# Kernel optimization log

Measured on AMD Instinct MI355X. Metric: run time of the kernel, lower is better.

The kernel has to match this reference:

```python
import jax, jax.numpy as jnp
import numpy as np

B_SZ, N_IN, N_CTX, UNITS, RANK = 4096, 4096, 512, 4096, 256


def setup_inputs() -> dict:
    key = jax.random.key(0)
    ks = jax.random.split(key, 8)
    inputs = jax.random.normal(ks[0], (B_SZ, N_IN), dtype=jnp.float32)
    context = jax.random.normal(ks[1], (B_SZ, N_CTX), dtype=jnp.float32)
    # Orthogonal-ish init approximated by scaled normals (math-equivalent shapes)
    U = jax.random.normal(ks[2], (N_IN, RANK), dtype=jnp.float32) / np.sqrt(N_IN)
    S = jax.random.uniform(ks[3], (RANK,), dtype=jnp.float32, minval=0.5, maxval=1.5)
    V = jax.random.normal(ks[4], (UNITS, RANK), dtype=jnp.float32) / np.sqrt(UNITS)
    W = jax.random.normal(ks[5], (N_CTX, RANK), dtype=jnp.float32) / np.sqrt(N_CTX)
    B = jnp.zeros((RANK,), dtype=jnp.float32)
    bias = jnp.zeros((UNITS,), dtype=jnp.float32)
    return {"inputs": inputs, "context": context, "U": U, "S": S, "V": V, "W": W, "B": B, "bias": bias}


def reference(inputs, context, U, S, V, W, B, bias):
    # chi[b,r] = sigmoid(context @ W + B)
    chi = jax.nn.sigmoid(context @ W + B)                  # [B, R]
    # Original: kernel[b,n,m] = sum_r U[n,r]*S[r]*chi[b,r]*V[m,r];
    # out[b,m] = sum_n x[b,n]*kernel[b,n,m]. Algebraically equal to:
    t = (inputs @ U) * (S * chi)                           # [B, R]
    out = t @ V.T + bias                                   # first '+ self.bias'
    out = out + bias                                       # 'outputs += self.bias' (use_bias=True)
    return jax.nn.relu(out)
```

## Files before the change

kernel.cpp:

```cpp
#include <hip/hip_runtime.h>

#define B_SZ 4096
#define N_IN 4096
#define N_CTX 512
#define UNITS 4096
#define RANK 256
#define ZSPLIT 16

typedef __attribute__((ext_vector_type(8))) __bf16 bf16x8;
typedef __attribute__((ext_vector_type(4))) float f32x4;
typedef __attribute__((ext_vector_type(8))) unsigned short ushort8;

__device__ __forceinline__ unsigned short f2bf(float f) {
    __bf16 h = (__bf16)f;
    return __builtin_bit_cast(unsigned short, h);
}
__device__ __forceinline__ float bf2f(unsigned short h) {
    return __uint_as_float(((unsigned int)h) << 16);
}
__device__ __forceinline__ void gload_lds16(const unsigned short* g, unsigned short* l) {
    __builtin_amdgcn_global_load_lds(
        (const __attribute__((address_space(1))) unsigned int*)g,
        (__attribute__((address_space(3))) unsigned int*)l, 16, 0, 0);
}
__device__ __forceinline__ bf16x8 ldfrag(const unsigned short* p) {
    ushort8 t = *(const ushort8*)p;
    return __builtin_bit_cast(bf16x8, t);
}

__global__ void prep(const float* __restrict__ U, const float* __restrict__ W,
                     const float* __restrict__ V,
                     unsigned short* __restrict__ UT, unsigned short* __restrict__ WT,
                     unsigned short* __restrict__ Vb) {
    __shared__ unsigned short t[64][66];
    int bid = blockIdx.x, tid = threadIdx.x;
    if (bid < 288) {
        const float* src; unsigned short* dst; int R, C, rb, cb;
        if (bid < 256) { src = U; dst = UT; R = N_IN; C = RANK; rb = (bid & 63) * 64; cb = (bid >> 6) * 64; }
        else { int b = bid - 256; src = W; dst = WT; R = N_CTX; C = RANK; rb = (b & 7) * 64; cb = (b >> 3) * 64; }
        int r = tid >> 4, c4 = (tid & 15) * 4;
        for (int i = 0; i < 4; i++) {
            float4 v = *(const float4*)(src + (size_t)(rb + r + i * 16) * C + cb + c4);
            t[r + i * 16][c4 + 0] = f2bf(v.x);
            t[r + i * 16][c4 + 1] = f2bf(v.y);
            t[r + i * 16][c4 + 2] = f2bf(v.z);
            t[r + i * 16][c4 + 3] = f2bf(v.w);
        }
        __syncthreads();
        int c = tid >> 3, r8 = (tid & 7) * 8;
        for (int j = 0; j < 2; j++) {
            int cc = c + j * 32;
            ushort8 o;
            for (int k = 0; k < 8; k++) o[k] = t[r8 + k][cc];
            *(ushort8*)(dst + (size_t)(cb + cc) * R + rb + r8) = o;
        }
    } else {
        size_t base = (size_t)(bid - 288) * 2048 + (size_t)tid * 8;
        float4 a = *(const float4*)(V + base);
        float4 b = *(const float4*)(V + base + 4);
        ushort8 o = { f2bf(a.x), f2bf(a.y), f2bf(a.z), f2bf(a.w),
                      f2bf(b.x), f2bf(b.y), f2bf(b.z), f2bf(b.w) };
        *(ushort8*)(Vb + base) = o;
    }
}


__launch_bounds__(512, 2)
__global__ void k21(const float* __restrict__ X, const unsigned short* __restrict__ UT,
                    unsigned short* __restrict__ T0p,
                    const float* __restrict__ ctx, const unsigned short* __restrict__ WT,
                    const float* __restrict__ S, const float* __restrict__ Bb,
                    unsigned short* __restrict__ Schi) {
    __shared__ char smem[49152];
    int tid = threadIdx.x, bfull = blockIdx.x;
    int w = tid >> 6, lane = tid & 63;
    int ln15 = lane & 15, quad = lane >> 4;
    if (bfull < 512) {
        int z = bfull >> 5, my = bfull & 31;
        unsigned short* As = (unsigned short*)smem;
        unsigned short* Bs = As + 128 * 64;
        int wr = w >> 2, wc = w & 3;
        int tm = my * 128;
        int kbase = z * (N_IN / ZSPLIT);
        f32x4 acc[4][4] = {};
        int arow = tid >> 2, acs0 = (tid & 3) * 2;
        const float* ag = X + (size_t)(tm + arow) * N_IN + kbase + acs0 * 8;
        unsigned short* al0 = As + arow * 64 + ((acs0 + 0) ^ (arow & 7)) * 8;
        unsigned short* al1 = As + arow * 64 + ((acs0 + 1) ^ (arow & 7)) * 8;
        int bl8 = lane >> 3, bcs = lane & 7;
        int bgc = (bcs ^ bl8) * 8;
        for (int kt = 0; kt < (N_IN / ZSPLIT) / 64; kt++) {
            int k0 = kt * 64;
            for (int c = 0; c < 4; c++) {
                int row = w * 32 + c * 8 + bl8;
                gload_lds16(UT + (size_t)row * N_IN + kbase + k0 + bgc, Bs + row * 64 + bcs * 8);
            }
            {
                float4 v0 = *(const float4*)(ag + k0);
                float4 v1 = *(const float4*)(ag + k0 + 4);
                float4 u0 = *(const float4*)(ag + k0 + 8);
                float4 u1 = *(const float4*)(ag + k0 + 12);
                ushort8 a8 = { f2bf(v0.x), f2bf(v0.y), f2bf(v0.z), f2bf(v0.w),
                               f2bf(v1.x), f2bf(v1.y), f2bf(v1.z), f2bf(v1.w) };
                ushort8 b8 = { f2bf(u0.x), f2bf(u0.y), f2bf(u0.z), f2bf(u0.w),
                               f2bf(u1.x), f2bf(u1.y), f2bf(u1.z), f2bf(u1.w) };
                *(ushort8*)al0 = a8;
                *(ushort8*)al1 = b8;
            }
            __syncthreads();
            for (int kh = 0; kh < 2; kh++) {
                int ch = kh * 4 + quad;
                int sw = (ch ^ (ln15 & 7)) * 8;
                bf16x8 af[4];
                for (int i = 0; i < 4; i++)
                    af[i] = ldfrag(As + (wr * 64 + i * 16 + ln15) * 64 + sw);
                for (int j = 0; j < 4; j++) {
                    bf16x8 b = ldfrag(Bs + (wc * 64 + j * 16 + ln15) * 64 + sw);
                    for (int i = 0; i < 4; i++)
                        acc[i][j] = __builtin_amdgcn_mfma_f32_16x16x32_bf16(af[i], b, acc[i][j], 0, 0, 0);
                }
            }
            __syncthreads();
        }
        unsigned short* P = T0p + (size_t)z * B_SZ * RANK;
        unsigned short* ep = (unsigned short*)smem;
        const int EPW = 280;
        int er = tid >> 3, ec0 = tid & 7;
        for (int h = 0; h < 2; h++) {
            if (wr == h) {
                for (int i = 0; i < 4; i++)
                    for (int j = 0; j < 4; j++)
                        for (int r = 0; r < 4; r++)
                            ep[(i * 16 + quad * 4 + r) * EPW + wc * 64 + j * 16 + ln15] = f2bf(acc[i][j][r]);
            }
            __syncthreads();
            for (int k = 0; k < 4; k++) {
                int chunk = ec0 + 8 * k;
                *(ushort8*)(P + (size_t)(tm + h * 64 + er) * RANK + chunk * 8) =
                    *(const ushort8*)(ep + er * EPW + chunk * 8);
            }
            __syncthreads();
        }
    } else {
        int hh = tid >> 8;
        int sb = (bfull - 512) * 2 + hh;
        int bx = sb & 3, by = sb >> 2;
        int t = tid & 255;
        int lw = t >> 6, llane = t & 63;
        int lln15 = llane & 15, lquad = llane >> 4;
        int wr = lw >> 1, wc = lw & 1;
        unsigned short* base = (unsigned short*)smem + hh * 6144;
        unsigned short* As = base;
        unsigned short* Bs = base + 32 * 64;
        int tm = by * 32, tn = bx * 64;
        f32x4 acc2[2] = {};
        int arow = t >> 3, acs = t & 7;
        const float* ag = ctx + (size_t)(tm + arow) * N_CTX + acs * 8;
        unsigned short* al = As + arow * 64 + (acs ^ (arow & 7)) * 8;
        int bl8 = llane >> 3, bcs = llane & 7;
        int bgc = (bcs ^ bl8) * 8;
        for (int kt = 0; kt < 8; kt++) {
            int k0 = kt * 64;
            for (int c = 0; c < 2; c++) {
                int row = lw * 16 + c * 8 + bl8;
                gload_lds16(WT + (size_t)(tn + row) * N_CTX + k0 + bgc, Bs + row * 64 + bcs * 8);
            }
            {
                float4 v0 = *(const float4*)(ag + k0);
                float4 v1 = *(const float4*)(ag + k0 + 4);
                ushort8 a8 = { f2bf(v0.x), f2bf(v0.y), f2bf(v0.z), f2bf(v0.w),
                               f2bf(v1.x), f2bf(v1.y), f2bf(v1.z), f2bf(v1.w) };
                *(ushort8*)al = a8;
            }
            __syncthreads();
            for (int kh = 0; kh < 2; kh++) {
                int ch = kh * 4 + lquad;
                bf16x8 af = ldfrag(As + (wr * 16 + lln15) * 64 + (ch ^ (lln15 & 7)) * 8);
                for (int j = 0; j < 2; j++) {
                    int row = wc * 32 + j * 16 + lln15;
                    bf16x8 bfr = ldfrag(Bs + row * 64 + (ch ^ (lln15 & 7)) * 8);
                    acc2[j] = __builtin_amdgcn_mfma_f32_16x16x32_bf16(af, bfr, acc2[j], 0, 0, 0);
                }
            }
            __syncthreads();
        }
        for (int j = 0; j < 2; j++) {
            int col = tn + wc * 32 + j * 16 + lln15;
            float sv = S[col], bv = Bb[col];
            for (int r = 0; r < 4; r++) {
                int row = tm + wr * 16 + lquad * 4 + r;
                float x = acc2[j][r] + bv;
                float chi = sv / (1.f + __expf(-x));
                Schi[(size_t)row * RANK + col] = f2bf(chi);
            }
        }
    }
}

__global__ void e_red(const unsigned short* __restrict__ T0p, const unsigned short* __restrict__ Schi,
                      unsigned short* __restrict__ T) {
    int i = blockIdx.x * 256 + threadIdx.x;
    const size_t stride = (size_t)B_SZ * RANK;
    float a[8] = {};
    for (int z = 0; z < ZSPLIT; z++) {
        ushort8 p = *(const ushort8*)(T0p + z * stride + (size_t)i * 8);
        for (int k = 0; k < 8; k++) a[k] += bf2f(p[k]);
    }
    ushort8 s = *(const ushort8*)(Schi + (size_t)i * 8);
    ushort8 o;
    for (int k = 0; k < 8; k++) o[k] = f2bf(a[k] * bf2f(s[k]));
    *(ushort8*)(T + (size_t)i * 8) = o;
}

__launch_bounds__(512, 1)
__global__ void k3_out(const unsigned short* __restrict__ T, const unsigned short* __restrict__ Vb,
                       const float* __restrict__ bias, float* __restrict__ out) {
    __shared__ char smem[163840];
    unsigned short* Bs = (unsigned short*)smem;
    unsigned short* A0 = (unsigned short*)(smem + 65536);
    unsigned short* A1 = A0 + 64 * 256;
    float* ep = (float*)(smem + 131072);
    int tid = threadIdx.x, w = tid >> 6, lane = tid & 63;
    int ln15 = lane & 15, quad = lane >> 4;
    int wr = w >> 2, wc = w & 3;
    int tn = blockIdx.x * 128;
    int tmg = blockIdx.y * 512;
    int lr2 = lane >> 5, lc16 = lane & 31;

    for (int i = 0; i < 8; i++) {
        int row = (w * 8 + i) * 2 + lr2;
        int g = (lc16 & 24) | ((lc16 & 7) ^ (row & 7));
        gload_lds16(Vb + (size_t)(tn + row) * RANK + g * 8, Bs + row * 256 + lc16 * 8);
    }
#define STAGE_A3(buf, step) do { \
    for (int i = 0; i < 4; i++) { \
        int row = (w * 4 + i) * 2 + lr2; \
        int g = (lc16 & 24) | ((lc16 & 7) ^ (row & 7)); \
        gload_lds16(T + (size_t)(tmg + (step) * 64 + row) * RANK + g * 8, \
                    (buf) + row * 256 + lc16 * 8); \
    } } while (0)
    STAGE_A3(A0, 0);
    float bv0 = 2.f * bias[tn + wc * 32 + ln15];
    float bv1 = 2.f * bias[tn + wc * 32 + 16 + ln15];
    unsigned short* cur = A0;
    unsigned short* nxt = A1;
    for (int t = 0; t < 8; t++) {
        STAGE_A3(nxt, (t + 1) & 7);
        asm volatile("s_waitcnt vmcnt(4)" ::: "memory");
        __builtin_amdgcn_s_barrier();
        __builtin_amdgcn_sched_barrier(0);
        f32x4 acc[2][2] = {};
        for (int kh = 0; kh < 8; kh++) {
            int c = kh * 4 + quad;
            bf16x8 af[2], bf[2];
            for (int i = 0; i < 2; i++) {
                int row = wr * 32 + i * 16 + ln15;
                int c16 = (c & 24) | ((c & 7) ^ (row & 7));
                af[i] = ldfrag(cur + row * 256 + c16 * 8);
            }
            for (int j = 0; j < 2; j++) {
                int row = wc * 32 + j * 16 + ln15;
                int c16 = (c & 24) | ((c & 7) ^ (row & 7));
                bf[j] = ldfrag(Bs + row * 256 + c16 * 8);
            }
            for (int i = 0; i < 2; i++)
                for (int j = 0; j < 2; j++)
                    acc[i][j] = __builtin_amdgcn_mfma_f32_16x16x32_bf16(af[i], bf[j], acc[i][j], 0, 0, 0);
        }
        for (int i = 0; i < 2; i++)
            for (int j = 0; j < 2; j++) {
                float bv = j ? bv1 : bv0;
                for (int r = 0; r < 4; r++)
                    ep[(wr * 32 + i * 16 + quad * 4 + r) * 128 + wc * 32 + j * 16 + ln15] =
                        fmaxf(acc[i][j][r] + bv, 0.f);
            }
        asm volatile("s_waitcnt lgkmcnt(0)" ::: "memory");
        __builtin_amdgcn_s_barrier();
        __builtin_amdgcn_sched_barrier(0);
        {
            int er = tid >> 3, ec = tid & 7;
            size_t orow = (size_t)(tmg + t * 64 + er) * UNITS + tn;
            for (int k = 0; k < 4; k++)
                *(float4*)(out + orow + (ec + k * 8) * 4) =
                    *(const float4*)(ep + er * 128 + (ec + k * 8) * 4);
        }
        __builtin_amdgcn_s_barrier();
        unsigned short* tmp = cur; cur = nxt; nxt = tmp;
    }
#undef STAGE_A3
}

extern "C" void kernel_launch(void* const* d_in, const int* in_sizes, int n_in,
                              void* d_out, int out_size, void* d_ws, size_t ws_size,
                              hipStream_t stream) {
    (void)in_sizes; (void)n_in; (void)out_size; (void)ws_size;
    const float* inputs  = (const float*)d_in[0];
    const float* context = (const float*)d_in[1];
    const float* U       = (const float*)d_in[2];
    const float* S       = (const float*)d_in[3];
    const float* V       = (const float*)d_in[4];
    const float* W       = (const float*)d_in[5];
    const float* Bb      = (const float*)d_in[6];
    const float* bias    = (const float*)d_in[7];
    float* out = (float*)d_out;

    char* ws = (char*)d_ws;
    size_t o = 0;
    unsigned short* UT   = (unsigned short*)(ws + o); o += (size_t)RANK * N_IN * 2;
    unsigned short* WT   = (unsigned short*)(ws + o); o += (size_t)RANK * N_CTX * 2;
    unsigned short* Vb   = (unsigned short*)(ws + o); o += (size_t)UNITS * RANK * 2;
    unsigned short* Schi = (unsigned short*)(ws + o); o += (size_t)B_SZ * RANK * 2;
    unsigned short* T    = (unsigned short*)(ws + o); o += (size_t)B_SZ * RANK * 2;
    unsigned short* T0p  = (unsigned short*)(ws + o); o += (size_t)ZSPLIT * B_SZ * RANK * 2;

    prep<<<800, 256, 0, stream>>>(U, W, V, UT, WT, Vb);
    k21<<<768, 512, 0, stream>>>(inputs, UT, T0p, context, WT, S, Bb, Schi);
    e_red<<<(B_SZ * RANK) / (256 * 8), 256, 0, stream>>>(T0p, Schi, T);
    k3_out<<<dim3(32, 8), 512, 0, stream>>>(T, Vb, bias, out);
}
```

Baseline: 176.5 us.

## Software-pipeline split-K GEMM with multi-buffered LDS and halve the K split

Rewrites the inputs@U split-K main loop as a software pipeline. B tiles are triple-buffered in LDS via direct global-to-LDS loads, and A tiles are double-buffered through registers with explicit vmcnt waits and raw barriers. MFMA priority is raised during compute. The K split drops from 16 to 8, so each block does twice the K work and the reduction has fewer partials to sum. The cost is 128KB of LDS per block at one block per CU, half as many GEMM blocks, and a fragile hand-written wait-count schedule.

```diff
diff --git a/kernel.cpp b/kernel.cpp
--- a/kernel.cpp
+++ b/kernel.cpp
@@ -5,7 +5,7 @@
 #define N_CTX 512
 #define UNITS 4096
 #define RANK 256
-#define ZSPLIT 16
+#define ZSPLIT 8
 
 typedef __attribute__((ext_vector_type(8))) __bf16 bf16x8;
 typedef __attribute__((ext_vector_type(4))) float f32x4;
@@ -26,6 +26,9 @@
 __device__ __forceinline__ bf16x8 ldfrag(const unsigned short* p) {
     ushort8 t = *(const ushort8*)p;
     return __builtin_bit_cast(bf16x8, t);
+}
+__device__ __forceinline__ void gld4(float4& d, const float* p) {
+    asm volatile("global_load_dwordx4 %0, %1, off" : "=v"(d) : "v"(p) : "memory");
 }
 
 __global__ void prep(const float* __restrict__ U, const float* __restrict__ W,
@@ -64,64 +67,111 @@
     }
 }
 
-
-__launch_bounds__(512, 2)
+__launch_bounds__(512, 1)
 __global__ void k21(const float* __restrict__ X, const unsigned short* __restrict__ UT,
                     unsigned short* __restrict__ T0p,
                     const float* __restrict__ ctx, const unsigned short* __restrict__ WT,
                     const float* __restrict__ S, const float* __restrict__ Bb,
                     unsigned short* __restrict__ Schi) {
-    __shared__ char smem[49152];
+    __shared__ char smem[131072];
     int tid = threadIdx.x, bfull = blockIdx.x;
     int w = tid >> 6, lane = tid & 63;
     int ln15 = lane & 15, quad = lane >> 4;
-    if (bfull < 512) {
-        int z = bfull >> 5, my = bfull & 31;
-        unsigned short* As = (unsigned short*)smem;
-        unsigned short* Bs = As + 128 * 64;
+    if (bfull < 256) {
+        int mblk = bfull & 31, z = bfull >> 5;
+        unsigned short* Bs = (unsigned short*)smem;
+        unsigned short* Al = Bs + 3 * 256 * 64;
         int wr = w >> 2, wc = w & 3;
-        int tm = my * 128;
+        int tm = mblk * 128;
         int kbase = z * (N_IN / ZSPLIT);
         f32x4 acc[4][4] = {};
+        int bl8 = lane >> 3, bcs = lane & 7;
+        int bgc = (bcs ^ bl8) * 8;
         int arow = tid >> 2, acs0 = (tid & 3) * 2;
         const float* ag = X + (size_t)(tm + arow) * N_IN + kbase + acs0 * 8;
-        unsigned short* al0 = As + arow * 64 + ((acs0 + 0) ^ (arow & 7)) * 8;
-        unsigned short* al1 = As + arow * 64 + ((acs0 + 1) ^ (arow & 7)) * 8;
-        int bl8 = lane >> 3, bcs = lane & 7;
-        int bgc = (bcs ^ bl8) * 8;
-        for (int kt = 0; kt < (N_IN / ZSPLIT) / 64; kt++) {
-            int k0 = kt * 64;
-            for (int c = 0; c < 4; c++) {
-                int row = w * 32 + c * 8 + bl8;
-                gload_lds16(UT + (size_t)row * N_IN + kbase + k0 + bgc, Bs + row * 64 + bcs * 8);
-            }
-            {
-                float4 v0 = *(const float4*)(ag + k0);
-                float4 v1 = *(const float4*)(ag + k0 + 4);
-                float4 u0 = *(const float4*)(ag + k0 + 8);
-                float4 u1 = *(const float4*)(ag + k0 + 12);
-                ushort8 a8 = { f2bf(v0.x), f2bf(v0.y), f2bf(v0.z), f2bf(v0.w),
-                               f2bf(v1.x), f2bf(v1.y), f2bf(v1.z), f2bf(v1.w) };
-                ushort8 b8 = { f2bf(u0.x), f2bf(u0.y), f2bf(u0.z), f2bf(u0.w),
-                               f2bf(u1.x), f2bf(u1.y), f2bf(u1.z), f2bf(u1.w) };
-                *(ushort8*)al0 = a8;
-                *(ushort8*)al1 = b8;
-            }
-            __syncthreads();
+        int aoff0 = arow * 64 + ((acs0 + 0) ^ (arow & 7)) * 8;
+        int aoff1 = arow * 64 + ((acs0 + 1) ^ (arow & 7)) * 8;
+        float4 ra[2][4];
+
+#define K2_B_STAGE(buf, k0) do { \
+    for (int c = 0; c < 4; c++) { \
+        int row = w * 32 + c * 8 + bl8; \
+        gload_lds16(UT + (size_t)row * N_IN + kbase + (k0) + bgc, \
+                    Bs + (buf) * 16384 + row * 64 + bcs * 8); \
+    } } while (0)
+#define K2_A_ISSUE(set, k0) do { \
+    gld4(ra[set][0], ag + (k0)); \
+    gld4(ra[set][1], ag + (k0) + 4); \
+    gld4(ra[set][2], ag + (k0) + 8); \
+    gld4(ra[set][3], ag + (k0) + 12); } while (0)
+#define K2_A_WRITE(set, buf) do { \
+    float4 x0 = ra[set][0], x1 = ra[set][1], x2 = ra[set][2], x3 = ra[set][3]; \
+    ushort8 o0 = { f2bf(x0.x), f2bf(x0.y), f2bf(x0.z), f2bf(x0.w), \
+                   f2bf(x1.x), f2bf(x1.y), f2bf(x1.z), f2bf(x1.w) }; \
+    ushort8 o1 = { f2bf(x2.x), f2bf(x2.y), f2bf(x2.z), f2bf(x2.w), \
+                   f2bf(x3.x), f2bf(x3.y), f2bf(x3.z), f2bf(x3.w) }; \
+    *(ushort8*)(Al + (buf) * 8192 + aoff0) = o0; \
+    *(ushort8*)(Al + (buf) * 8192 + aoff1) = o1; } while (0)
+#define WAITV(n) do { \
+    asm volatile("s_waitcnt vmcnt(" #n ")" ::: "memory"); \
+    __builtin_amdgcn_sched_barrier(0); } while (0)
+#define WAITL0 do { \
+    asm volatile("s_waitcnt lgkmcnt(0)" ::: "memory"); \
+    __builtin_amdgcn_sched_barrier(0); } while (0)
+
+        K2_A_ISSUE(0, 0);
+        K2_B_STAGE(0, 0);
+        K2_B_STAGE(1, 64);
+        WAITV(8);
+        K2_A_WRITE(0, 0);
+        K2_A_ISSUE(1, 64);
+        WAITV(8);
+        WAITL0;
+        __builtin_amdgcn_s_barrier();
+        __builtin_amdgcn_sched_barrier(0);
+
+#pragma unroll
+        for (int t = 0; t < 8; t++) {
+            if (t + 2 < 8) {
+                K2_A_ISSUE(t & 1, (t + 2) * 64);
+                K2_B_STAGE((t + 2) % 3, (t + 2) * 64);
+            }
+            __builtin_amdgcn_s_setprio(1);
+#pragma unroll
             for (int kh = 0; kh < 2; kh++) {
                 int ch = kh * 4 + quad;
                 int sw = (ch ^ (ln15 & 7)) * 8;
                 bf16x8 af[4];
+#pragma unroll
                 for (int i = 0; i < 4; i++)
-                    af[i] = ldfrag(As + (wr * 64 + i * 16 + ln15) * 64 + sw);
+                    af[i] = ldfrag(Al + (t & 1) * 8192 + (wr * 64 + i * 16 + ln15) * 64 + sw);
+#pragma unroll
                 for (int j = 0; j < 4; j++) {
-                    bf16x8 b = ldfrag(Bs + (wc * 64 + j * 16 + ln15) * 64 + sw);
+                    bf16x8 b = ldfrag(Bs + (t % 3) * 16384 + (wc * 64 + j * 16 + ln15) * 64 + sw);
+#pragma unroll
                     for (int i = 0; i < 4; i++)
                         acc[i][j] = __builtin_amdgcn_mfma_f32_16x16x32_bf16(af[i], b, acc[i][j], 0, 0, 0);
                 }
             }
-            __syncthreads();
-        }
+            __builtin_amdgcn_s_setprio(0);
+            if (t < 7) {
+                if (t + 2 < 8) {
+                    WAITV(8);
+                } else {
+                    WAITV(0);
+                }
+                K2_A_WRITE((t + 1) & 1, (t + 1) & 1);
+                WAITL0;
+                __builtin_amdgcn_s_barrier();
+                __builtin_amdgcn_sched_barrier(0);
+            }
+        }
+#undef K2_B_STAGE
+#undef K2_A_ISSUE
+#undef K2_A_WRITE
+#undef WAITV
+#undef WAITL0
+        __syncthreads();
         unsigned short* P = T0p + (size_t)z * B_SZ * RANK;
         unsigned short* ep = (unsigned short*)smem;
         const int EPW = 280;
@@ -143,7 +193,7 @@
         }
     } else {
         int hh = tid >> 8;
-        int sb = (bfull - 512) * 2 + hh;
+        int sb = (bfull - 256) * 2 + hh;
         int bx = sb & 3, by = sb >> 2;
         int t = tid & 255;
         int lw = t >> 6, llane = t & 63;
@@ -314,7 +364,7 @@
     unsigned short* T0p  = (unsigned short*)(ws + o); o += (size_t)ZSPLIT * B_SZ * RANK * 2;
 
     prep<<<800, 256, 0, stream>>>(U, W, V, UT, WT, Vb);
-    k21<<<768, 512, 0, stream>>>(inputs, UT, T0p, context, WT, S, Bb, Schi);
+    k21<<<512, 512, 0, stream>>>(inputs, UT, T0p, context, WT, S, Bb, Schi);
     e_red<<<(B_SZ * RANK) / (256 * 8), 256, 0, stream>>>(T0p, Schi, T);
     k3_out<<<dim3(32, 8), 512, 0, stream>>>(T, Vb, bias, out);
 }
```

Result: faster. 170.2 us (-3.6%).
